# Kernel tuning notes

Hardware: AMD Instinct MI355X
Metric: run time of the kernel (lower is better)

Reference implementation:

```python
import jax, jax.numpy as jnp
import numpy as np

WS = 8          # window size
NH = 8          # num heads
DIM = 256
HD = DIM // NH  # head dim = 32
SCALE = HD ** -0.5
EPS = 1e-5


def _rel_pos_index(ws):
    # deterministic int index buffer, same math as the torch __init__
    coords = jnp.stack(jnp.meshgrid(jnp.arange(ws), jnp.arange(ws), indexing='ij'))  # [2,ws,ws]
    cf = coords.reshape(2, -1)                     # [2, N]
    rel = cf[:, :, None] - cf[:, None, :]          # [2, N, N]
    return (rel[0] + ws - 1) * (2 * ws - 1) + (rel[1] + ws - 1)  # [N, N]


def _ln(h, g, b):
    m = jnp.mean(h, axis=-1, keepdims=True)
    v = jnp.mean((h - m) ** 2, axis=-1, keepdims=True)
    return (h - m) / jnp.sqrt(v + EPS) * g + b


def setup_inputs() -> dict:
    key = jax.random.key(0)
    ks = jax.random.split(key, 16)
    B_, N, D = 4096, WS * WS, DIM
    s = 0.02
    return {
        'x':      jax.random.normal(ks[0], (B_, N, D), jnp.float32),
        # enhanced qkv: Linear(D,2D) -> LN -> GELU -> Linear(2D,3D)
        'w_qkv1': jax.random.normal(ks[1], (D, 2 * D), jnp.float32) * s,
        'b_qkv1': jnp.zeros((2 * D,), jnp.float32),
        'g_qkv':  jnp.ones((2 * D,), jnp.float32),
        'be_qkv': jnp.zeros((2 * D,), jnp.float32),
        'w_qkv2': jax.random.normal(ks[2], (2 * D, 3 * D), jnp.float32) * s,
        'b_qkv2': jnp.zeros((3 * D,), jnp.float32),
        # relative position bias table [(2*WS-1)^2, NH]
        'rpb':    jax.random.normal(ks[3], ((2 * WS - 1) ** 2, NH), jnp.float32) * s,
        # enhanced proj: Linear(D,2D) -> LN -> GELU -> Linear(2D,D)
        'w_p1':   jax.random.normal(ks[4], (D, 2 * D), jnp.float32) * s,
        'b_p1':   jnp.zeros((2 * D,), jnp.float32),
        'g_p':    jnp.ones((2 * D,), jnp.float32),
        'be_p':   jnp.zeros((2 * D,), jnp.float32),
        'w_p2':   jax.random.normal(ks[5], (2 * D, D), jnp.float32) * s,
        'b_p2':   jnp.zeros((D,), jnp.float32),
    }


def reference(x, w_qkv1, b_qkv1, g_qkv, be_qkv, w_qkv2, b_qkv2, rpb,
              w_p1, b_p1, g_p, be_p, w_p2, b_p2):
    B_, N, C = x.shape
    # enhanced QKV chain: Linear -> LayerNorm -> GELU -> Linear
    h = jax.nn.gelu(_ln(x @ w_qkv1 + b_qkv1, g_qkv, be_qkv), approximate=False)
    qkv = h @ w_qkv2 + b_qkv2                              # [B_, N, 3C]
    qkv = qkv.reshape(B_, N, 3, NH, HD).transpose(2, 0, 3, 1, 4)  # [3, B_, H, N, hd]
    q, k, v = qkv[0], qkv[1], qkv[2]
    attn = jnp.einsum('bhnd,bhmd->bhnm', q * SCALE, k)     # [B_, H, N, N]
    idx = _rel_pos_index(WS)                                # [N, N] int
    bias = rpb[idx.reshape(-1)].reshape(N, N, NH).transpose(2, 0, 1)  # [H, N, N]
    attn = jax.nn.softmax(attn + bias[None], axis=-1)
    out = jnp.einsum('bhnm,bhmd->bhnd', attn, v)           # [B_, H, N, hd]
    out = out.transpose(0, 2, 1, 3).reshape(B_, N, C)
    # enhanced proj chain: Linear -> LayerNorm -> GELU -> Linear
    h = jax.nn.gelu(_ln(out @ w_p1 + b_p1, g_p, be_p), approximate=False)
    return h @ w_p2 + b_p2
```

## Files before the change

### kernel.cpp

```cpp
#include <hip/hip_runtime.h>


typedef __bf16 bf16_t;
typedef __bf16 bf16x8 __attribute__((ext_vector_type(8)));
typedef __bf16 bf16x4 __attribute__((ext_vector_type(4)));
typedef float f32x4 __attribute__((ext_vector_type(4)));

__device__ __forceinline__ f32x4 mfma16(bf16x8 a, bf16x8 b, f32x4 acc) {
  return __builtin_amdgcn_mfma_f32_16x16x32_bf16(a, b, acc, 0, 0, 0);
}

#define SWZ(row, byteoff) ((byteoff) ^ (((row) & 7) << 4))

__device__ __forceinline__ float gelu_f(float v) {
  float e = __expf(v * (1.59576912f + 0.07135482f * v * v));
  return v - v * __builtin_amdgcn_rcpf(1.0f + e);
}

__global__ void wtrans_kernel(const float* __restrict__ src, bf16_t* __restrict__ dst,
                              int kshift, int N, int total) {
  int i = blockIdx.x * 256 + threadIdx.x;
  if (i >= total) return;
  int K = 1 << kshift;
  int k = i & (K - 1);
  int n = i >> kshift;
  dst[i] = (bf16_t)src[(size_t)k * N + n];
}

__global__ void biastab_kernel(const float* __restrict__ rpb, float* __restrict__ bt) {
  int e = blockIdx.x * 256 + threadIdx.x;
  int hd = e >> 12, i = (e >> 6) & 63, j = e & 63;
  int idx = ((i >> 3) - (j >> 3) + 7) * 15 + ((i & 7) - (j & 7) + 7);
  bt[e] = rpb[idx * 8 + hd];
}

__device__ __forceinline__ void gemmT_ln_gelu(
    const char* bsrc, const bf16_t* __restrict__ wt,
    const float* __restrict__ bias, const float* __restrict__ gamma,
    const float* __restrict__ beta,
    char* dst, int flb, float2* part, int wave, int g, int c)
{
  f32x4 acc[4][4] = {};
#pragma unroll
  for (int kt = 0; kt < 8; ++kt) {
    bf16x8 a[4], b[4];
#pragma unroll
    for (int mt = 0; mt < 4; ++mt)
      a[mt] = *(const bf16x8*)(wt + (size_t)(wave * 64 + mt * 16 + c) * 256 + kt * 32 + g * 8);
#pragma unroll
    for (int nt = 0; nt < 4; ++nt) {
      int T = nt * 16 + c;
      b[nt] = *(const bf16x8*)(bsrc + SWZ(T, T * 512 + kt * 64 + g * 16));
    }
#pragma unroll
    for (int mt = 0; mt < 4; ++mt)
#pragma unroll
      for (int nt = 0; nt < 4; ++nt)
        acc[mt][nt] = mfma16(a[mt], b[nt], acc[mt][nt]);
  }
  float s[4] = {0.f, 0.f, 0.f, 0.f}, ss[4] = {0.f, 0.f, 0.f, 0.f};
#pragma unroll
  for (int mt = 0; mt < 4; ++mt) {
    float4 b4 = *(const float4*)(bias + wave * 64 + mt * 16 + g * 4);
#pragma unroll
    for (int nt = 0; nt < 4; ++nt)
#pragma unroll
      for (int r = 0; r < 4; ++r) {
        float v = acc[mt][nt][r] + ((const float*)&b4)[r];
        acc[mt][nt][r] = v;
        s[nt] += v;
        ss[nt] += v * v;
      }
  }
#pragma unroll
  for (int nt = 0; nt < 4; ++nt) {
    float sv = s[nt], ssv = ss[nt];
    sv += __shfl_xor(sv, 16, 64); ssv += __shfl_xor(ssv, 16, 64);
    sv += __shfl_xor(sv, 32, 64); ssv += __shfl_xor(ssv, 32, 64);
    if (g == 0) part[wave * 64 + nt * 16 + c] = make_float2(sv, ssv);
  }
  __syncthreads();
#pragma unroll
  for (int nt = 0; nt < 4; ++nt) {
    float sv = 0.f, ssv = 0.f;
#pragma unroll
    for (int w = 0; w < 8; ++w) {
      float2 p2 = part[w * 64 + nt * 16 + c];
      sv += p2.x; ssv += p2.y;
    }
    float m = sv * (1.f / 512.f);
    float rstd = rsqrtf(ssv * (1.f / 512.f) - m * m + 1e-5f);
#pragma unroll
    for (int mt = 0; mt < 4; ++mt)
#pragma unroll
      for (int r = 0; r < 4; ++r)
        acc[mt][nt][r] = (acc[mt][nt][r] - m) * rstd;
  }
#pragma unroll
  for (int mt = 0; mt < 4; ++mt) {
    float4 g4 = *(const float4*)(gamma + wave * 64 + mt * 16 + g * 4);
    float4 be4 = *(const float4*)(beta + wave * 64 + mt * 16 + g * 4);
    int f0 = flb + mt * 16 + g * 4;
#pragma unroll
    for (int nt = 0; nt < 4; ++nt) {
      int T = nt * 16 + c;
      bf16x4 h4;
#pragma unroll
      for (int r = 0; r < 4; ++r) {
        float v = acc[mt][nt][r] * ((const float*)&g4)[r] + ((const float*)&be4)[r];
        h4[r] = (bf16_t)gelu_f(v);
      }
      *(bf16x4*)(dst + SWZ(T, T * 512 + f0 * 2)) = h4;
    }
  }
}

__global__ __launch_bounds__(512, 2) void g1qa_kernel(
    const float* __restrict__ x,
    const bf16_t* __restrict__ w1t, const float* __restrict__ b1,
    const float* __restrict__ gamma1, const float* __restrict__ beta1,
    const bf16_t* __restrict__ w2t, const float* __restrict__ b2,
    const float* __restrict__ bt,
    bf16_t* __restrict__ ao)
{
  __shared__ __align__(16) char sm[81920];
  char* rA = sm;
  char* rB = sm + 32768;
  char* ded = sm + 65536;
  float2* part = (float2*)ded;
  const int tid = threadIdx.x;
  const int wave = tid >> 6, lane = tid & 63;
  const int g = lane >> 4, c = lane & 15;
  const int win = blockIdx.x;
  const int head = wave;

  const float* xw = x + (size_t)win * 16384;
#pragma unroll
  for (int it = 0; it < 8; ++it) {
    int e = it * 2048 + tid * 4;
    float4 v = *(const float4*)(xw + e);
    int row = e >> 8, col = e & 255;
    bf16x4 t4;
    t4[0] = (bf16_t)v.x; t4[1] = (bf16_t)v.y; t4[2] = (bf16_t)v.z; t4[3] = (bf16_t)v.w;
    *(bf16x4*)(rA + SWZ(row, row * 512 + col * 2)) = t4;
  }
  __syncthreads();
  gemmT_ln_gelu(rA, w1t, b1, gamma1, beta1, (wave < 4) ? rB : rA, (wave & 3) * 64,
                part, wave, g, c);
  __syncthreads();

  bf16x4 vreg[2][4], qreg[2][4], kreg[2][4];

  {
    f32x4 acc[2][4] = {};
#pragma unroll
    for (int kt = 0; kt < 16; ++kt) {
      const char* hb = (kt < 8) ? rB : rA;
      const int ko = (kt & 7) * 64 + g * 16;
      bf16x8 a[2], b[4];
#pragma unroll
      for (int mt = 0; mt < 2; ++mt)
        a[mt] = *(const bf16x8*)(w2t + (size_t)(512 + head * 32 + mt * 16 + c) * 512 + kt * 32 + g * 8);
#pragma unroll
      for (int nt = 0; nt < 4; ++nt) {
        int T = nt * 16 + c;
        b[nt] = *(const bf16x8*)(hb + SWZ(T, T * 512 + ko));
      }
#pragma unroll
      for (int mt = 0; mt < 2; ++mt)
#pragma unroll
        for (int nt = 0; nt < 4; ++nt)
          acc[mt][nt] = mfma16(a[mt], b[nt], acc[mt][nt]);
    }
    if (head < 4) {
      char* vs = ded + head * 4096;
#pragma unroll
      for (int mt = 0; mt < 2; ++mt) {
        float4 b4 = *(const float4*)(b2 + 512 + head * 32 + mt * 16 + g * 4);
#pragma unroll
        for (int nt = 0; nt < 4; ++nt) {
          int T = nt * 16 + c;
#pragma unroll
          for (int r = 0; r < 4; ++r) {
            int d = mt * 16 + g * 4 + r;
            *(bf16_t*)(vs + SWZ(d, d * 128 + T * 2)) =
                (bf16_t)(acc[mt][nt][r] + ((const float*)&b4)[r]);
          }
        }
      }
    } else {
#pragma unroll
      for (int mt = 0; mt < 2; ++mt) {
        float4 b4 = *(const float4*)(b2 + 512 + head * 32 + mt * 16 + g * 4);
#pragma unroll
        for (int nt = 0; nt < 4; ++nt) {
          bf16x4 o4;
#pragma unroll
          for (int r = 0; r < 4; ++r)
            o4[r] = (bf16_t)(acc[mt][nt][r] + ((const float*)&b4)[r]);
          vreg[mt][nt] = o4;
        }
      }
    }
  }
  {
    f32x4 acc[2][4] = {};
#pragma unroll
    for (int kt = 0; kt < 16; ++kt) {
      const char* hb = (kt < 8) ? rB : rA;
      const int ko = (kt & 7) * 64 + g * 16;
      bf16x8 a[2], b[4];
#pragma unroll
      for (int mt = 0; mt < 2; ++mt)
        a[mt] = *(const bf16x8*)(w2t + (size_t)(head * 32 + mt * 16 + c) * 512 + kt * 32 + g * 8);
#pragma unroll
      for (int nt = 0; nt < 4; ++nt) {
        int T = nt * 16 + c;
        b[nt] = *(const bf16x8*)(hb + SWZ(T, T * 512 + ko));
      }
#pragma unroll
      for (int mt = 0; mt < 2; ++mt)
#pragma unroll
        for (int nt = 0; nt < 4; ++nt)
          acc[mt][nt] = mfma16(a[mt], b[nt], acc[mt][nt]);
    }
#pragma unroll
    for (int mt = 0; mt < 2; ++mt) {
      float4 b4 = *(const float4*)(b2 + head * 32 + mt * 16 + g * 4);
#pragma unroll
      for (int nt = 0; nt < 4; ++nt) {
        bf16x4 o4;
#pragma unroll
        for (int r = 0; r < 4; ++r)
          o4[r] = (bf16_t)((acc[mt][nt][r] + ((const float*)&b4)[r]) * 0.17677669529663687f);
        qreg[mt][nt] = o4;
      }
    }
  }
  {
    f32x4 acc[2][4] = {};
#pragma unroll
    for (int kt = 0; kt < 16; ++kt) {
      const char* hb = (kt < 8) ? rB : rA;
      const int ko = (kt & 7) * 64 + g * 16;
      bf16x8 a[2], b[4];
#pragma unroll
      for (int mt = 0; mt < 2; ++mt)
        a[mt] = *(const bf16x8*)(w2t + (size_t)(256 + head * 32 + mt * 16 + c) * 512 + kt * 32 + g * 8);
#pragma unroll
      for (int nt = 0; nt < 4; ++nt) {
        int T = nt * 16 + c;
        b[nt] = *(const bf16x8*)(hb + SWZ(T, T * 512 + ko));
      }
#pragma unroll
      for (int mt = 0; mt < 2; ++mt)
#pragma unroll
        for (int nt = 0; nt < 4; ++nt)
          acc[mt][nt] = mfma16(a[mt], b[nt], acc[mt][nt]);
    }
#pragma unroll
    for (int mt = 0; mt < 2; ++mt) {
      float4 b4 = *(const float4*)(b2 + 256 + head * 32 + mt * 16 + g * 4);
#pragma unroll
      for (int nt = 0; nt < 4; ++nt) {
        bf16x4 o4;
#pragma unroll
        for (int r = 0; r < 4; ++r)
          o4[r] = (bf16_t)(acc[mt][nt][r] + ((const float*)&b4)[r]);
        kreg[mt][nt] = o4;
      }
    }
  }
  __syncthreads();

  {
    char* qb = sm + (head & 3) * 8192 + (head >> 2) * 32768;
#pragma unroll
    for (int mt = 0; mt < 2; ++mt)
#pragma unroll
      for (int nt = 0; nt < 4; ++nt) {
        int T = nt * 16 + c, d0 = mt * 16 + g * 4;
        *(bf16x4*)(qb + SWZ(T, T * 64 + d0 * 2)) = qreg[mt][nt];
        *(bf16x4*)(qb + 4096 + SWZ(T, T * 64 + d0 * 2)) = kreg[mt][nt];
      }
  }
  __syncthreads();

  const int rowbase = (wave >> 2) * 32;
#pragma unroll
  for (int s = 0; s < 2; ++s) {
    const int hd = s * 4 + (wave & 3);
    char* qb = sm + (wave & 3) * 8192 + s * 32768;
    char* vslot = ded + (wave & 3) * 4096;
    const float* btab = bt + hd * 4096;

    bf16x8 aq[2], bk[4];
#pragma unroll
    for (int mt = 0; mt < 2; ++mt) {
      int t = rowbase + mt * 16 + c;
      aq[mt] = *(const bf16x8*)(qb + SWZ(t, t * 64 + g * 16));
    }
#pragma unroll
    for (int nt = 0; nt < 4; ++nt) {
      int t = nt * 16 + c;
      bk[nt] = *(const bf16x8*)(qb + 4096 + SWZ(t, t * 64 + g * 16));
    }
    float p[2][4][4];
#pragma unroll
    for (int mt = 0; mt < 2; ++mt)
#pragma unroll
      for (int nt = 0; nt < 4; ++nt) {
        f32x4 z = {0.f, 0.f, 0.f, 0.f};
        f32x4 s4 = mfma16(aq[mt], bk[nt], z);
#pragma unroll
        for (int r = 0; r < 4; ++r) {
          int i = rowbase + mt * 16 + g * 4 + r, j = nt * 16 + c;
          p[mt][nt][r] = s4[r] + btab[i * 64 + j];
        }
      }
#pragma unroll
    for (int mt = 0; mt < 2; ++mt)
#pragma unroll
      for (int r = 0; r < 4; ++r) {
        float mx = fmaxf(fmaxf(p[mt][0][r], p[mt][1][r]), fmaxf(p[mt][2][r], p[mt][3][r]));
#pragma unroll
        for (int m = 1; m < 16; m <<= 1) mx = fmaxf(mx, __shfl_xor(mx, m, 64));
        float sum = 0.f;
#pragma unroll
        for (int nt = 0; nt < 4; ++nt) {
          float e = __expf(p[mt][nt][r] - mx);
          p[mt][nt][r] = e; sum += e;
        }
#pragma unroll
        for (int m = 1; m < 16; m <<= 1) sum += __shfl_xor(sum, m, 64);
        float rinv = 1.f / sum;
#pragma unroll
        for (int nt = 0; nt < 4; ++nt) p[mt][nt][r] *= rinv;
      }
    __syncthreads();
#pragma unroll
    for (int mt = 0; mt < 2; ++mt)
#pragma unroll
      for (int nt = 0; nt < 4; ++nt)
#pragma unroll
        for (int r = 0; r < 4; ++r) {
          int i = rowbase + mt * 16 + g * 4 + r, j = nt * 16 + c;
          *(bf16_t*)(qb + SWZ(i, i * 128 + j * 2)) = (bf16_t)p[mt][nt][r];
        }
    asm volatile("s_waitcnt lgkmcnt(0)" ::: "memory");
    f32x4 oacc[2][2] = {};
#pragma unroll
    for (int kp = 0; kp < 2; ++kp) {
      bf16x8 ap[2], bv[2];
#pragma unroll
      for (int mt = 0; mt < 2; ++mt) {
        int t = rowbase + mt * 16 + c;
        ap[mt] = *(const bf16x8*)(qb + SWZ(t, t * 128 + kp * 64 + g * 16));
      }
#pragma unroll
      for (int nt = 0; nt < 2; ++nt) {
        int d = nt * 16 + c;
        bv[nt] = *(const bf16x8*)(vslot + SWZ(d, d * 128 + kp * 64 + g * 16));
      }
#pragma unroll
      for (int mt = 0; mt < 2; ++mt)
#pragma unroll
        for (int nt = 0; nt < 2; ++nt)
          oacc[mt][nt] = mfma16(ap[mt], bv[nt], oacc[mt][nt]);
    }
#pragma unroll
    for (int mt = 0; mt < 2; ++mt)
#pragma unroll
      for (int nt = 0; nt < 2; ++nt)
#pragma unroll
        for (int r = 0; r < 4; ++r) {
          int T = rowbase + mt * 16 + g * 4 + r;
          ao[(size_t)(win * 64 + T) * 256 + hd * 32 + nt * 16 + c] = (bf16_t)oacc[mt][nt][r];
        }
    __syncthreads();
    if (s == 0) {
      if (head >= 4) {
        char* vs = ded + (head & 3) * 4096;
#pragma unroll
        for (int mt = 0; mt < 2; ++mt)
#pragma unroll
          for (int nt = 0; nt < 4; ++nt) {
            int T = nt * 16 + c;
#pragma unroll
            for (int r = 0; r < 4; ++r) {
              int d = mt * 16 + g * 4 + r;
              *(bf16_t*)(vs + SWZ(d, d * 128 + T * 2)) = vreg[mt][nt][r];
            }
          }
      }
      __syncthreads();
    }
  }
}

__global__ __launch_bounds__(512, 2) void g3g4_kernel(
    const bf16_t* __restrict__ ao,
    const bf16_t* __restrict__ wp1t, const float* __restrict__ bp1,
    const float* __restrict__ gp, const float* __restrict__ bep,
    const bf16_t* __restrict__ wp2t, const float* __restrict__ bp2,
    float* __restrict__ out)
{
  __shared__ __align__(16) char sm[69632];
  char* rA = sm;
  char* rB = sm + 32768;
  float2* part = (float2*)(sm + 65536);
  const int tid = threadIdx.x;
  const int wave = tid >> 6, lane = tid & 63;
  const int g = lane >> 4, c = lane & 15;
  const int win = blockIdx.x;

  const bf16_t* aow = ao + (size_t)win * 16384;
#pragma unroll
  for (int it = 0; it < 4; ++it) {
    int e = it * 4096 + tid * 8;
    bf16x8 v = *(const bf16x8*)(aow + e);
    int row = e >> 8, col = e & 255;
    *(bf16x8*)(rA + SWZ(row, row * 512 + col * 2)) = v;
  }
  __syncthreads();
  gemmT_ln_gelu(rA, wp1t, bp1, gp, bep, (wave < 4) ? rB : rA, (wave & 3) * 64,
                part, wave, g, c);
  __syncthreads();

  f32x4 acc[2][4] = {};
#pragma unroll
  for (int kt = 0; kt < 16; ++kt) {
    const char* hb = (kt < 8) ? rB : rA;
    const int ko = (kt & 7) * 64 + g * 16;
    bf16x8 a[2], b[4];
#pragma unroll
    for (int mt = 0; mt < 2; ++mt)
      a[mt] = *(const bf16x8*)(wp2t + (size_t)(wave * 32 + mt * 16 + c) * 512 + kt * 32 + g * 8);
#pragma unroll
    for (int nt = 0; nt < 4; ++nt) {
      int T = nt * 16 + c;
      b[nt] = *(const bf16x8*)(hb + SWZ(T, T * 512 + ko));
    }
#pragma unroll
    for (int mt = 0; mt < 2; ++mt)
#pragma unroll
      for (int nt = 0; nt < 4; ++nt)
        acc[mt][nt] = mfma16(a[mt], b[nt], acc[mt][nt]);
  }
  float* ow = out + (size_t)win * 16384;
#pragma unroll
  for (int mt = 0; mt < 2; ++mt) {
    float4 b4 = *(const float4*)(bp2 + wave * 32 + mt * 16 + g * 4);
#pragma unroll
    for (int nt = 0; nt < 4; ++nt) {
      int T = nt * 16 + c;
      f32x4 o4;
#pragma unroll
      for (int r = 0; r < 4; ++r) o4[r] = acc[mt][nt][r] + ((const float*)&b4)[r];
      *(f32x4*)(ow + T * 256 + wave * 32 + mt * 16 + g * 4) = o4;
    }
  }
}

extern "C" void kernel_launch(void* const* d_in, const int* in_sizes, int n_in,
                              void* d_out, int out_size, void* d_ws, size_t ws_size,
                              hipStream_t stream) {
  const float* x   = (const float*)d_in[0];
  const float* w1  = (const float*)d_in[1];
  const float* b1  = (const float*)d_in[2];
  const float* g1  = (const float*)d_in[3];
  const float* be1 = (const float*)d_in[4];
  const float* w2  = (const float*)d_in[5];
  const float* b2  = (const float*)d_in[6];
  const float* rpb = (const float*)d_in[7];
  const float* wp1 = (const float*)d_in[8];
  const float* bp1 = (const float*)d_in[9];
  const float* gp  = (const float*)d_in[10];
  const float* bep = (const float*)d_in[11];
  const float* wp2 = (const float*)d_in[12];
  const float* bp2 = (const float*)d_in[13];
  float* out = (float*)d_out;
  char* ws = (char*)d_ws;
  bf16_t* w1t  = (bf16_t*)(ws + 0);
  bf16_t* w2t  = (bf16_t*)(ws + 262144);
  bf16_t* wp1t = (bf16_t*)(ws + 1048576);
  bf16_t* wp2t = (bf16_t*)(ws + 1310720);
  float*  bt   = (float*)(ws + 1572864);
  bf16_t* ao   = (bf16_t*)(ws + 2097152);

  wtrans_kernel<<<512, 256, 0, stream>>>(w1, w1t, 8, 512, 131072);
  wtrans_kernel<<<1536, 256, 0, stream>>>(w2, w2t, 9, 768, 393216);
  wtrans_kernel<<<512, 256, 0, stream>>>(wp1, wp1t, 8, 512, 131072);
  wtrans_kernel<<<512, 256, 0, stream>>>(wp2, wp2t, 9, 256, 131072);
  biastab_kernel<<<128, 256, 0, stream>>>(rpb, bt);

  g1qa_kernel<<<4096, 512, 0, stream>>>(x, w1t, b1, g1, be1, w2t, b2, bt, ao);
  g3g4_kernel<<<4096, 512, 0, stream>>>(ao, wp1t, bp1, gp, bep, wp2t, bp2, out);
}
```

Baseline: 1.156 ms.

## Shrink attention kernel LDS by relocating V and staging Q/K per half

Removes the dedicated 16 KB V region from the fused QKV+attention kernel's shared memory, cutting the allocation from 80 KB to 68 KB. All eight heads now write V into the freed rB region at once. Q/K staging is split so heads 0-3 write before the first attention pass and heads 4-7 reuse the same slots before the second. The smaller LDS footprint is meant to let more blocks fit per CU. In exchange, heads 4-7 keep Q/K in registers longer, and the synchronisation points are rearranged.

```diff
diff --git a/kernel.cpp b/kernel.cpp
--- a/kernel.cpp
+++ b/kernel.cpp
@@ -123,11 +123,10 @@
     const float* __restrict__ bt,
     bf16_t* __restrict__ ao)
 {
-  __shared__ __align__(16) char sm[81920];
+  __shared__ __align__(16) char sm[69632];
   char* rA = sm;
   char* rB = sm + 32768;
-  char* ded = sm + 65536;
-  float2* part = (float2*)ded;
+  float2* part = (float2*)(sm + 65536);
   const int tid = threadIdx.x;
   const int wave = tid >> 6, lane = tid & 63;
   const int g = lane >> 4, c = lane & 15;
@@ -172,34 +171,16 @@
         for (int nt = 0; nt < 4; ++nt)
           acc[mt][nt] = mfma16(a[mt], b[nt], acc[mt][nt]);
     }
-    if (head < 4) {
-      char* vs = ded + head * 4096;
-#pragma unroll
-      for (int mt = 0; mt < 2; ++mt) {
-        float4 b4 = *(const float4*)(b2 + 512 + head * 32 + mt * 16 + g * 4);
-#pragma unroll
-        for (int nt = 0; nt < 4; ++nt) {
-          int T = nt * 16 + c;
-#pragma unroll
-          for (int r = 0; r < 4; ++r) {
-            int d = mt * 16 + g * 4 + r;
-            *(bf16_t*)(vs + SWZ(d, d * 128 + T * 2)) =
-                (bf16_t)(acc[mt][nt][r] + ((const float*)&b4)[r]);
-          }
-        }
-      }
-    } else {
-#pragma unroll
-      for (int mt = 0; mt < 2; ++mt) {
-        float4 b4 = *(const float4*)(b2 + 512 + head * 32 + mt * 16 + g * 4);
-#pragma unroll
-        for (int nt = 0; nt < 4; ++nt) {
-          bf16x4 o4;
-#pragma unroll
-          for (int r = 0; r < 4; ++r)
-            o4[r] = (bf16_t)(acc[mt][nt][r] + ((const float*)&b4)[r]);
-          vreg[mt][nt] = o4;
-        }
+#pragma unroll
+    for (int mt = 0; mt < 2; ++mt) {
+      float4 b4 = *(const float4*)(b2 + 512 + head * 32 + mt * 16 + g * 4);
+#pragma unroll
+      for (int nt = 0; nt < 4; ++nt) {
+        bf16x4 o4;
+#pragma unroll
+        for (int r = 0; r < 4; ++r)
+          o4[r] = (bf16_t)(acc[mt][nt][r] + ((const float*)&b4)[r]);
+        vreg[mt][nt] = o4;
       }
     }
   }
@@ -274,7 +255,21 @@
   __syncthreads();
 
   {
-    char* qb = sm + (head & 3) * 8192 + (head >> 2) * 32768;
+    char* vs = sm + 32768 + (head >> 2) * 16384 + (head & 3) * 4096;
+#pragma unroll
+    for (int mt = 0; mt < 2; ++mt)
+#pragma unroll
+      for (int nt = 0; nt < 4; ++nt) {
+        int T = nt * 16 + c;
+#pragma unroll
+        for (int r = 0; r < 4; ++r) {
+          int d = mt * 16 + g * 4 + r;
+          *(bf16_t*)(vs + SWZ(d, d * 128 + T * 2)) = vreg[mt][nt][r];
+        }
+      }
+  }
+  if (head < 4) {
+    char* qb = sm + head * 8192;
 #pragma unroll
     for (int mt = 0; mt < 2; ++mt)
 #pragma unroll
@@ -284,14 +279,26 @@
         *(bf16x4*)(qb + 4096 + SWZ(T, T * 64 + d0 * 2)) = kreg[mt][nt];
       }
   }
-  __syncthreads();
 
   const int rowbase = (wave >> 2) * 32;
 #pragma unroll
   for (int s = 0; s < 2; ++s) {
+    if (s == 1 && head >= 4) {
+      char* qb = sm + (head & 3) * 8192;
+#pragma unroll
+      for (int mt = 0; mt < 2; ++mt)
+#pragma unroll
+        for (int nt = 0; nt < 4; ++nt) {
+          int T = nt * 16 + c, d0 = mt * 16 + g * 4;
+          *(bf16x4*)(qb + SWZ(T, T * 64 + d0 * 2)) = qreg[mt][nt];
+          *(bf16x4*)(qb + 4096 + SWZ(T, T * 64 + d0 * 2)) = kreg[mt][nt];
+        }
+    }
+    __syncthreads();
+
     const int hd = s * 4 + (wave & 3);
-    char* qb = sm + (wave & 3) * 8192 + s * 32768;
-    char* vslot = ded + (wave & 3) * 4096;
+    char* qb = sm + (wave & 3) * 8192;
+    char* vslot = sm + 32768 + s * 16384 + (wave & 3) * 4096;
     const float* btab = bt + hd * 4096;
 
     bf16x8 aq[2], bk[4];
@@ -377,24 +384,7 @@
           int T = rowbase + mt * 16 + g * 4 + r;
           ao[(size_t)(win * 64 + T) * 256 + hd * 32 + nt * 16 + c] = (bf16_t)oacc[mt][nt][r];
         }
-    __syncthreads();
-    if (s == 0) {
-      if (head >= 4) {
-        char* vs = ded + (head & 3) * 4096;
-#pragma unroll
-        for (int mt = 0; mt < 2; ++mt)
-#pragma unroll
-          for (int nt = 0; nt < 4; ++nt) {
-            int T = nt * 16 + c;
-#pragma unroll
-            for (int r = 0; r < 4; ++r) {
-              int d = mt * 16 + g * 4 + r;
-              *(bf16_t*)(vs + SWZ(d, d * 128 + T * 2)) = vreg[mt][nt][r];
-            }
-          }
-      }
-      __syncthreads();
-    }
+    if (s == 0) __syncthreads();
   }
 }
 
```

After: 1.201 ms. 1.04x slower.
